# Performance work log

Measured on AMD Instinct MI355X. Metric: run time of the kernel, lower is better.

Reference implementation:

```python
import jax, jax.numpy as jnp
import numpy as np

S, B, T = 500, 128, 250          # encoder steps, batch, decoder text_len
H, K, V, VOCAB = 512, 128, 128, 1000
NEG = -1e9


def _lstm_cell(x, h, c, w_ih, w_hh, b_ih, b_hh):
    # torch.nn.LSTMCell gate order: i, f, g, o
    gates = x @ w_ih.T + b_ih + h @ w_hh.T + b_hh
    i, f, g, o = jnp.split(gates, 4, axis=-1)
    c_new = jax.nn.sigmoid(f) * c + jax.nn.sigmoid(i) * jnp.tanh(g)
    h_new = jax.nn.sigmoid(o) * jnp.tanh(c_new)
    return h_new, c_new


def setup_inputs():
    root = jax.random.key(0)
    ks = jax.random.split(root, 12)
    w = lambda k, shape, fan: (jax.random.normal(k, shape, jnp.float32) / np.sqrt(fan))
    inp = {
        'key': jax.random.normal(ks[0], (S, B, K), jnp.float32),
        'values': jax.random.normal(ks[1], (S, B, V), jnp.float32),
        'lens': jnp.maximum(jax.random.randint(ks[2], (B,), 0, S), 1),
        'text': jax.random.randint(ks[3], (T, B), 0, VOCAB),
        # embedding, padding_idx=0 -> row 0 zeroed
        'emb': w(ks[4], (VOCAB, H), H).at[0].set(0.0),
        # lstm1: input hidden_dim + value_size -> hidden H
        'w_ih1': w(ks[5], (4 * H, H + V), H + V),
        'w_hh1': w(ks[6], (4 * H, H), H),
        'b_ih1': jnp.zeros((4 * H,), jnp.float32),
        'b_hh1': jnp.zeros((4 * H,), jnp.float32),
        # lstm2: input H -> key_size K
        'w_ih2': w(ks[7], (4 * K, H), H),
        'w_hh2': w(ks[8], (4 * K, K), K),
        'b_ih2': jnp.zeros((4 * K,), jnp.float32),
        'b_hh2': jnp.zeros((4 * K,), jnp.float32),
        # character_prob: (key_size+value_size) -> vocab
        'w_out': w(ks[9], (VOCAB, K + V), K + V),
        'b_out': jnp.zeros((VOCAB,), jnp.float32),
    }
    return inp


def reference(key, values, lens, text, emb, w_ih1, w_hh1, b_ih1, b_hh1,
              w_ih2, w_hh2, b_ih2, b_hh2, w_out, b_out):
    key_t = jnp.transpose(key, (1, 0, 2))      # [B,S,K]
    val_t = jnp.transpose(values, (1, 0, 2))   # [B,S,V]
    mask = jnp.arange(S)[None, :] >= lens[:, None]  # [B,S] True = padded

    # teacher forcing ratio == 1: step 0 uses embedding(argmax(zeros)) = row 0,
    # steps i>=1 use embeddings[i]. Precompute the whole input sequence.
    embs = emb[text]  # [T,B,H]
    step0 = jnp.broadcast_to(emb[0], (1, B, H))
    char_seq = jnp.concatenate([step0, embs[1:T - 1]], axis=0)  # [T-1,B,H]

    def step(carry, char_embed):
        h1, c1, h2, c2, context = carry
        inp = jnp.concatenate([char_embed, context], axis=1)        # [B,H+V]
        h1, c1 = _lstm_cell(inp, h1, c1, w_ih1, w_hh1, b_ih1, b_hh1)
        h2, c2 = _lstm_cell(h1, h2, c2, w_ih2, w_hh2, b_ih2, b_hh2)  # query [B,K]
        energy = jnp.einsum('bsk,bk->bs', key_t, h2)
        energy = jnp.where(mask, NEG, energy)
        attn = jax.nn.softmax(energy, axis=1)
        context = jnp.einsum('bs,bsv->bv', attn, val_t)              # [B,V]
        pred = jnp.concatenate([h2, context], axis=1) @ w_out.T + b_out
        return (h1, c1, h2, c2, context), pred

    z = lambda d: jnp.zeros((B, d), jnp.float32)
    init = (z(H), z(H), z(K), z(K), z(V))
    _, preds = jax.lax.scan(step, init, char_seq)   # [T-1,B,VOCAB]
    return jnp.transpose(preds, (1, 0, 2))          # [B,T-1,VOCAB]
```

## Files before the change

kernel.cpp:

```cpp
#include <hip/hip_runtime.h>
#include <hip/hip_bf16.h>

typedef unsigned short u16;
typedef unsigned long long u64;
typedef short short8 __attribute__((ext_vector_type(8)));
typedef float f32x4 __attribute__((ext_vector_type(4)));

#define S_ 500
#define B_ 128
#define T_ 250
#define H_ 512
#define K_ 128
#define V_ 128
#define VOC 1000
#define NSTEP 249
#define NWG 160
#define NROW 128

#define VSH_BYTES   128000
#define H1ST_STRIDE 520
#define ALIAS_BYTES 33280
#define SMEM_BYTES  (VSH_BYTES + ALIAS_BYTES)

__device__ __forceinline__ float bf2f(u16 u) {
    union { unsigned int i; float f; } x; x.i = ((unsigned int)u) << 16; return x.f;
}
__device__ __forceinline__ u16 f2bf(float f) {
    union { float f; unsigned int i; } x; x.f = f;
    unsigned int r = x.i + 0x7fffu + ((x.i >> 16) & 1u);
    return (u16)(r >> 16);
}
__device__ __forceinline__ float sigm(float x) { return 1.f / (1.f + __expf(-x)); }
__device__ __forceinline__ f32x4 mfma16(short8 a, short8 b, f32x4 c) {
    return __builtin_amdgcn_mfma_f32_16x16x32_bf16(a, b, c, 0, 0, 0);
}

__device__ __forceinline__ u64 ld_state8(const u16* p) {
    return __hip_atomic_load((const u64*)p, __ATOMIC_RELAXED, __HIP_MEMORY_SCOPE_AGENT);
}
__device__ __forceinline__ short8 ld_state16(const u16* p) {
    union { u64 q[2]; short8 s; } u;
    u.q[0] = ld_state8(p); u.q[1] = ld_state8(p + 4);
    return u.s;
}
__device__ __forceinline__ unsigned ld_state4(const u16* p) {
    return __hip_atomic_load((const unsigned*)p, __ATOMIC_RELAXED, __HIP_MEMORY_SCOPE_AGENT);
}
__device__ __forceinline__ void st_state4(u16* p, unsigned v) {
    __hip_atomic_store((unsigned*)p, v, __ATOMIC_RELAXED, __HIP_MEMORY_SCOPE_AGENT);
}
__device__ __forceinline__ void st_pair(u16* p, float a, float b) {
    st_state4(p, (unsigned)f2bf(a) | ((unsigned)f2bf(b) << 16));
}

__device__ __forceinline__ void gbar(unsigned* bar, int wg) {
    __syncthreads();
    if (threadIdx.x == 0) {
        unsigned* leaf = bar + (wg & 7) * 64;
        unsigned* root = bar + 512;
        unsigned* gen  = bar + 576;
        unsigned g = __hip_atomic_load(gen, __ATOMIC_RELAXED, __HIP_MEMORY_SCOPE_AGENT);
        unsigned a = __hip_atomic_fetch_add(leaf, 1u, __ATOMIC_RELAXED, __HIP_MEMORY_SCOPE_AGENT);
        if (a == 19u) {
            __hip_atomic_store(leaf, 0u, __ATOMIC_RELAXED, __HIP_MEMORY_SCOPE_AGENT);
            unsigned r = __hip_atomic_fetch_add(root, 1u, __ATOMIC_RELAXED, __HIP_MEMORY_SCOPE_AGENT);
            if (r == 7u) {
                __hip_atomic_store(root, 0u, __ATOMIC_RELAXED, __HIP_MEMORY_SCOPE_AGENT);
                __hip_atomic_store(gen, g + 1u, __ATOMIC_RELAXED, __HIP_MEMORY_SCOPE_AGENT);
            } else {
                while (__hip_atomic_load(gen, __ATOMIC_RELAXED, __HIP_MEMORY_SCOPE_AGENT) == g)
                    __builtin_amdgcn_s_sleep(1);
            }
        } else {
            while (__hip_atomic_load(gen, __ATOMIC_RELAXED, __HIP_MEMORY_SCOPE_AGENT) == g)
                __builtin_amdgcn_s_sleep(1);
        }
    }
    __syncthreads();
}

__global__ __launch_bounds__(256) void pack_kernel(
    const float* __restrict__ w_ih1, const float* __restrict__ w_hh1,
    const float* __restrict__ b_ih1, const float* __restrict__ b_hh1,
    const float* __restrict__ w_ih2, const float* __restrict__ w_hh2,
    const float* __restrict__ b_ih2, const float* __restrict__ b_hh2,
    const float* __restrict__ w_out, const float* __restrict__ emb,
    u16* __restrict__ W1f, u16* __restrict__ W2f, u16* __restrict__ Woutf,
    float* __restrict__ bias1, float* __restrict__ bias2, u16* __restrict__ emb_bf,
    unsigned* __restrict__ bar)
{
    const int i0 = blockIdx.x * 256 + threadIdx.x;
    const int stride = gridDim.x * 256;
    for (int i = i0; i < 1024; i += stride)
        __hip_atomic_store(bar + i, 0u, __ATOMIC_RELAXED, __HIP_MEMORY_SCOPE_AGENT);
    for (int i = i0; i < 1152 * 2048; i += stride) {
        int k = i >> 11, n = i & 2047;
        float v = (k < 640) ? w_ih1[n * 640 + k] : w_hh1[n * 512 + (k - 640)];
        W1f[((size_t)(k >> 3) * 2048 + n) * 8 + (k & 7)] = f2bf(v);
    }
    for (int i = i0; i < 640 * 512; i += stride) {
        int k = i >> 9, n = i & 511;
        float v = (k < 512) ? w_ih2[n * 512 + k] : w_hh2[n * 128 + (k - 512)];
        W2f[((size_t)(k >> 3) * 512 + n) * 8 + (k & 7)] = f2bf(v);
    }
    for (int i = i0; i < 256 * 1024; i += stride) {
        int k = i >> 10, n = i & 1023;
        float v = (n < VOC) ? w_out[n * 256 + k] : 0.f;
        Woutf[((size_t)(k >> 3) * 1024 + n) * 8 + (k & 7)] = f2bf(v);
    }
    for (int i = i0; i < 2048; i += stride) bias1[i] = b_ih1[i] + b_hh1[i];
    for (int i = i0; i < 512; i += stride) bias2[i] = b_ih2[i] + b_hh2[i];
    for (int i = i0; i < VOC * H_; i += stride) emb_bf[i] = f2bf(emb[i]);
}

__global__ __launch_bounds__(256) void conv_kv_kernel(
    const float* __restrict__ key, const float* __restrict__ values,
    u16* __restrict__ key_bf, u16* __restrict__ val_bf)
{
    const int i0 = blockIdx.x * 256 + threadIdx.x;
    const int stride = gridDim.x * 256;
    for (int i = i0; i < S_ * B_ * K_; i += stride) {
        int s = i >> 14;
        int r = i & 16383;
        int b = r >> 7, k = r & 127;
        size_t d = ((size_t)b * S_ + s) * K_ + k;
        key_bf[d] = f2bf(key[i]);
        val_bf[d] = f2bf(values[i]);
    }
}

__global__ __launch_bounds__(256, 1) void decoder_kernel(
    const u16* __restrict__ emb_bf, const int* __restrict__ text,
    const u16* __restrict__ W1f, const float* __restrict__ bias1,
    const u16* __restrict__ W2f, const float* __restrict__ bias2,
    const u16* __restrict__ key_bf, const u16* __restrict__ val_bf,
    const int* __restrict__ lens,
    u16* __restrict__ CT, u16* __restrict__ H1, u16* __restrict__ H2,
    u16* __restrict__ Hc, unsigned* __restrict__ bar)
{
    extern __shared__ char smem[];
    u16*   vshare = (u16*)smem;
    char*  alias  = smem + VSH_BYTES;
    u16*   h1st   = (u16*)alias;
    float* Gb     = (float*)alias;
    float* ebuf   = (float*)alias;
    float* cbuf   = (float*)(alias + 2048);
    float* h2s    = (float*)(alias + 4096);
    float* redm   = (float*)(alias + 4608);

    const int wg = blockIdx.x;
    const int tid = threadIdx.x;
    const int lane = tid & 63, wv = tid >> 6;
    const int lrow = lane & 15, lk = lane >> 4;
    const bool isrow = wg < NROW;

    const int mh1 = wg >> 5, hg1 = wg & 31;
    const int n1 = wv * 512 + hg1 * 16 + lrow;
    const int l2 = wg - NROW;
    const int q2 = l2 >> 3, hg2 = l2 & 7;
    const int n2 = wv * 128 + hg2 * 16 + lrow;
    const int b  = wg;
    const int mylen = isrow ? lens[b] : 0;

    float c1r[2] = {0.f, 0.f};
    float c2r[2] = {0.f, 0.f};
    f32x4 acc1[2] = {{0,0,0,0},{0,0,0,0}};
    f32x4 acc2[2] = {{0,0,0,0},{0,0,0,0}};

    {
        int i0 = wg * 256 + tid, stride = NWG * 256;
        for (int i = i0; i < B_ * V_ / 2; i += stride) st_state4(CT + 2 * i, 0u);
        for (int i = i0; i < B_ * H_ / 2; i += stride) st_state4(H1 + 2 * i, 0u);
        for (int i = i0; i < B_ * K_;     i += stride) st_state4(H2 + 2 * i, 0u);
        if (isrow) {
            const u16* vp = val_bf + (size_t)b * S_ * V_;
            for (int i = tid; i < (S_ * V_) / 8; i += 256)
                *reinterpret_cast<short8*>(vshare + i * 8) =
                    *reinterpret_cast<const short8*>(vp + (size_t)i * 8);
        }
    }
    gbar(bar, wg);

    for (int t = 0; t < NSTEP; ++t) {
        const int nxt = (t & 1) ^ 1;
        u16* H2n = H2 + (size_t)nxt * B_ * K_;

        if (isrow) {
            int grow[2];
#pragma unroll
            for (int rt = 0; rt < 2; ++rt) grow[rt] = mh1 * 32 + rt * 16 + lrow;
#pragma unroll
            for (int kc = 16; kc < 20; ++kc) {
                int k = kc * 32 + lk * 8;
                short8 bw = *reinterpret_cast<const short8*>(W1f + ((size_t)(k >> 3) * 2048 + n1) * 8);
#pragma unroll
                for (int rt = 0; rt < 2; ++rt) {
                    short8 a = ld_state16(CT + grow[rt] * V_ + (k - 512));
                    acc1[rt] = mfma16(a, bw, acc1[rt]);
                }
            }
            float bv = bias1[n1];
#pragma unroll
            for (int rt = 0; rt < 2; ++rt)
#pragma unroll
                for (int j = 0; j < 4; ++j)
                    Gb[(rt * 16 + lk * 4 + j) * 65 + wv * 16 + lrow] = acc1[rt][j] + bv;
            __syncthreads();
            {
                int rb = tid >> 3, j0 = (tid & 7) * 2;
                int bb = mh1 * 32 + rb;
                float gi0 = Gb[rb * 65 + j0],      gf0 = Gb[rb * 65 + 16 + j0];
                float gg0 = Gb[rb * 65 + 32 + j0], go0 = Gb[rb * 65 + 48 + j0];
                float gi1 = Gb[rb * 65 + j0 + 1],      gf1 = Gb[rb * 65 + 16 + j0 + 1];
                float gg1 = Gb[rb * 65 + 32 + j0 + 1], go1 = Gb[rb * 65 + 48 + j0 + 1];
                float cn0 = sigm(gf0) * c1r[0] + sigm(gi0) * tanhf(gg0);
                float cn1 = sigm(gf1) * c1r[1] + sigm(gi1) * tanhf(gg1);
                c1r[0] = cn0; c1r[1] = cn1;
                st_pair(H1 + bb * H_ + hg1 * 16 + j0,
                        sigm(go0) * tanhf(cn0), sigm(go1) * tanhf(cn1));
            }
        }
        gbar(bar, wg);

        if (isrow) {
            {
                const u16* src = H1 + (size_t)(mh1 * 32) * H_;
#pragma unroll
                for (int it = 0; it < 8; ++it) {
                    int c = it * 256 + tid;
                    int row = c >> 6, col = (c & 63) * 8;
                    u64 lo = ld_state8(src + (size_t)row * H_ + col);
                    u64 hi = ld_state8(src + (size_t)row * H_ + col + 4);
                    u64* dst = (u64*)(h1st + row * H1ST_STRIDE + col);
                    dst[0] = lo; dst[1] = hi;
                }
            }
            const u16* aemb[2];
#pragma unroll
            for (int rt = 0; rt < 2; ++rt) {
                int grow = mh1 * 32 + rt * 16 + lrow;
                int tok = text[(t + 1) * B_ + grow];
                aemb[rt] = emb_bf + (size_t)tok * H_;
            }
            __syncthreads();
            acc1[0] = (f32x4){0,0,0,0}; acc1[1] = (f32x4){0,0,0,0};
#pragma unroll 4
            for (int kc = 0; kc < 16; ++kc) {
                int k = kc * 32 + lk * 8;
                short8 bw = *reinterpret_cast<const short8*>(W1f + ((size_t)(k >> 3) * 2048 + n1) * 8);
#pragma unroll
                for (int rt = 0; rt < 2; ++rt) {
                    short8 a = *reinterpret_cast<const short8*>(aemb[rt] + k);
                    acc1[rt] = mfma16(a, bw, acc1[rt]);
                }
            }
#pragma unroll 4
            for (int kc = 20; kc < 36; ++kc) {
                int k = kc * 32 + lk * 8;
                short8 bw = *reinterpret_cast<const short8*>(W1f + ((size_t)(k >> 3) * 2048 + n1) * 8);
#pragma unroll
                for (int rt = 0; rt < 2; ++rt) {
                    short8 a = *reinterpret_cast<const short8*>(
                        h1st + (rt * 16 + lrow) * H1ST_STRIDE + (kc - 20) * 32 + lk * 8);
                    acc1[rt] = mfma16(a, bw, acc1[rt]);
                }
            }
        } else {
            {
                const u16* src = H1 + (size_t)(q2 * 32) * H_;
#pragma unroll
                for (int it = 0; it < 8; ++it) {
                    int c = it * 256 + tid;
                    int row = c >> 6, col = (c & 63) * 8;
                    u64 lo = ld_state8(src + (size_t)row * H_ + col);
                    u64 hi = ld_state8(src + (size_t)row * H_ + col + 4);
                    u64* dst = (u64*)(h1st + row * H1ST_STRIDE + col);
                    dst[0] = lo; dst[1] = hi;
                }
            }
            __syncthreads();
#pragma unroll 4
            for (int kc = 0; kc < 16; ++kc) {
                int k = kc * 32 + lk * 8;
                short8 bw = *reinterpret_cast<const short8*>(W2f + ((size_t)(k >> 3) * 512 + n2) * 8);
#pragma unroll
                for (int rt = 0; rt < 2; ++rt) {
                    short8 a = *reinterpret_cast<const short8*>(
                        h1st + (rt * 16 + lrow) * H1ST_STRIDE + kc * 32 + lk * 8);
                    acc2[rt] = mfma16(a, bw, acc2[rt]);
                }
            }
            float bv = bias2[n2];
            __syncthreads();
#pragma unroll
            for (int rt = 0; rt < 2; ++rt)
#pragma unroll
                for (int j = 0; j < 4; ++j)
                    Gb[(rt * 16 + lk * 4 + j) * 65 + wv * 16 + lrow] = acc2[rt][j] + bv;
            __syncthreads();
            {
                int rb = tid >> 3, j0 = (tid & 7) * 2;
                int bb = q2 * 32 + rb;
                float gi0 = Gb[rb * 65 + j0],      gf0 = Gb[rb * 65 + 16 + j0];
                float gg0 = Gb[rb * 65 + 32 + j0], go0 = Gb[rb * 65 + 48 + j0];
                float gi1 = Gb[rb * 65 + j0 + 1],      gf1 = Gb[rb * 65 + 16 + j0 + 1];
                float gg1 = Gb[rb * 65 + 32 + j0 + 1], go1 = Gb[rb * 65 + 48 + j0 + 1];
                float cn0 = sigm(gf0) * c2r[0] + sigm(gi0) * tanhf(gg0);
                float cn1 = sigm(gf1) * c2r[1] + sigm(gi1) * tanhf(gg1);
                c2r[0] = cn0; c2r[1] = cn1;
                st_pair(H2n + bb * K_ + hg2 * 16 + j0,
                        sigm(go0) * tanhf(cn0), sigm(go1) * tanhf(cn1));
            }
        }
        gbar(bar, wg);

        if (isrow) {
            u16* Hc_t = Hc + (size_t)t * B_ * 256;
            if (tid < 64) {
                unsigned v = ld_state4(H2n + b * K_ + 2 * tid);
                h2s[2 * tid]     = bf2f((u16)(v & 0xffffu));
                h2s[2 * tid + 1] = bf2f((u16)(v >> 16));
                *reinterpret_cast<unsigned*>(Hc_t + b * 256 + 2 * tid) = v;
            }
            __syncthreads();

            for (int s = tid; s < 512; s += 256) {
                float e = -1e9f;
                if (s < S_) {
                    const u16* kp = key_bf + ((size_t)b * S_ + s) * K_;
                    float a = 0.f;
#pragma unroll
                    for (int kk = 0; kk < K_; kk += 8) {
                        short8 kv = *reinterpret_cast<const short8*>(kp + kk);
#pragma unroll
                        for (int j = 0; j < 8; ++j)
                            a += bf2f((u16)kv[j]) * h2s[kk + j];
                    }
                    e = (s < mylen) ? a : -1e9f;
                }
                ebuf[s] = e;
            }
            __syncthreads();

            float m = fmaxf(ebuf[tid], ebuf[tid + 256]);
#pragma unroll
            for (int off = 32; off > 0; off >>= 1) m = fmaxf(m, __shfl_down(m, off));
            if (lane == 0) redm[wv] = m;
            __syncthreads();
            const float maxv = fmaxf(fmaxf(redm[0], redm[1]), fmaxf(redm[2], redm[3]));

            float psum = 0.f;
            for (int s = tid; s < 512; s += 256) {
                float pv = __expf(ebuf[s] - maxv);
                ebuf[s] = pv;
                psum += pv;
            }
#pragma unroll
            for (int off = 32; off > 0; off >>= 1) psum += __shfl_down(psum, off);
            if (lane == 0) redm[4 + wv] = psum;
            __syncthreads();
            const float rinv = 1.f / (redm[4] + redm[5] + redm[6] + redm[7]);

            const int s0 = wv * 125;
            float p0 = 0.f, p1 = 0.f;
            for (int s = s0; s < s0 + 125; ++s) {
                float w = ebuf[s];
                unsigned pk = *reinterpret_cast<const unsigned*>(vshare + s * V_ + lane * 2);
                p0 += w * bf2f((u16)(pk & 0xffffu));
                p1 += w * bf2f((u16)(pk >> 16));
            }
            cbuf[wv * V_ + lane * 2]     = p0;
            cbuf[wv * V_ + lane * 2 + 1] = p1;
            __syncthreads();

            if (tid < 64) {
                int v0 = 2 * tid, v1 = 2 * tid + 1;
                float ctx0 = (cbuf[v0] + cbuf[V_ + v0] + cbuf[2 * V_ + v0] + cbuf[3 * V_ + v0]) * rinv;
                float ctx1 = (cbuf[v1] + cbuf[V_ + v1] + cbuf[2 * V_ + v1] + cbuf[3 * V_ + v1]) * rinv;
                st_pair(CT + b * V_ + v0, ctx0, ctx1);
                *reinterpret_cast<unsigned*>(Hc_t + b * 256 + K_ + v0) =
                    (unsigned)f2bf(ctx0) | ((unsigned)f2bf(ctx1) << 16);
            }
        } else {
            acc2[0] = (f32x4){0,0,0,0}; acc2[1] = (f32x4){0,0,0,0};
#pragma unroll
            for (int kc = 16; kc < 20; ++kc) {
                int k = kc * 32 + lk * 8;
                short8 bw = *reinterpret_cast<const short8*>(W2f + ((size_t)(k >> 3) * 512 + n2) * 8);
#pragma unroll
                for (int rt = 0; rt < 2; ++rt) {
                    short8 a = ld_state16(H2n + (q2 * 32 + rt * 16 + lrow) * K_ + (k - 512));
                    acc2[rt] = mfma16(a, bw, acc2[rt]);
                }
            }
        }
        gbar(bar, wg);
    }
}

__global__ __launch_bounds__(256) void k4_kernel(
    const u16* __restrict__ Hc, const u16* __restrict__ Woutf,
    const float* __restrict__ b_out, float* __restrict__ out)
{
    const int bx = blockIdx.x;
    const int mt = bx >> 4, nt = bx & 15;
    const int tid = threadIdx.x;
    const int lane = tid & 63, g = tid >> 6;
    const int lrow = lane & 15, lk = lane >> 4;
    const int n = nt * 64 + g * 16 + lrow;
    const float bias = (n < VOC) ? b_out[n] : 0.f;

    f32x4 acc[8];
#pragma unroll
    for (int rt = 0; rt < 8; ++rt) acc[rt] = (f32x4){bias, bias, bias, bias};

#pragma unroll
    for (int kc = 0; kc < 8; ++kc) {
        int k = kc * 32 + lk * 8;
        short8 bw = *reinterpret_cast<const short8*>(Woutf + ((size_t)(k >> 3) * 1024 + n) * 8);
#pragma unroll
        for (int rt = 0; rt < 8; ++rt) {
            int R = mt * 128 + rt * 16 + lrow;
            short8 a = *reinterpret_cast<const short8*>(Hc + (size_t)R * 256 + k);
            acc[rt] = mfma16(a, bw, acc[rt]);
        }
    }
    if (n < VOC) {
#pragma unroll
        for (int rt = 0; rt < 8; ++rt)
#pragma unroll
            for (int j = 0; j < 4; ++j) {
                int R = mt * 128 + rt * 16 + lk * 4 + j;
                int tt = R >> 7, bb = R & 127;
                out[((size_t)bb * NSTEP + tt) * VOC + n] = acc[rt][j];
            }
    }
}

extern "C" void kernel_launch(void* const* d_in, const int* in_sizes, int n_in,
                              void* d_out, int out_size, void* d_ws, size_t ws_size,
                              hipStream_t stream)
{
    const float* key    = (const float*)d_in[0];
    const float* values = (const float*)d_in[1];
    const int*   lens   = (const int*)d_in[2];
    const int*   text   = (const int*)d_in[3];
    const float* emb    = (const float*)d_in[4];
    const float* w_ih1  = (const float*)d_in[5];
    const float* w_hh1  = (const float*)d_in[6];
    const float* b_ih1  = (const float*)d_in[7];
    const float* b_hh1  = (const float*)d_in[8];
    const float* w_ih2  = (const float*)d_in[9];
    const float* w_hh2  = (const float*)d_in[10];
    const float* b_ih2  = (const float*)d_in[11];
    const float* b_hh2  = (const float*)d_in[12];
    const float* w_out  = (const float*)d_in[13];
    const float* b_out  = (const float*)d_in[14];

    char* p = (char*)d_ws;
    auto alloc = [&](size_t bytes) -> char* {
        char* r = p;
        p += (bytes + 255) & ~(size_t)255;
        return r;
    };
    u16*      key_bf = (u16*)     alloc((size_t)B_ * S_ * K_ * 2);
    u16*      val_bf = (u16*)     alloc((size_t)B_ * S_ * V_ * 2);
    u16*      emb_bf = (u16*)     alloc((size_t)VOC * H_ * 2);
    u16*      W1f    = (u16*)     alloc((size_t)1152 * 2048 * 2);
    u16*      W2f    = (u16*)     alloc((size_t)640 * 512 * 2);
    u16*      Woutf  = (u16*)     alloc((size_t)256 * 1024 * 2);
    float*    bias1  = (float*)   alloc(2048 * 4);
    float*    bias2  = (float*)   alloc(512 * 4);
    u16*      CT     = (u16*)     alloc((size_t)B_ * V_ * 2);
    u16*      H1     = (u16*)     alloc((size_t)B_ * H_ * 2);
    u16*      H2     = (u16*)     alloc((size_t)2 * B_ * K_ * 2);
    u16*      Hc     = (u16*)     alloc((size_t)NSTEP * B_ * 256 * 2);
    unsigned* bar    = (unsigned*)alloc(4096);
    (void)ws_size; (void)in_sizes; (void)n_in; (void)out_size;

    hipFuncSetAttribute((const void*)decoder_kernel,
                        hipFuncAttributeMaxDynamicSharedMemorySize, SMEM_BYTES);

    pack_kernel<<<512, 256, 0, stream>>>(w_ih1, w_hh1, b_ih1, b_hh1,
                                         w_ih2, w_hh2, b_ih2, b_hh2,
                                         w_out, emb, W1f, W2f, Woutf, bias1, bias2, emb_bf,
                                         bar);
    conv_kv_kernel<<<4096, 256, 0, stream>>>(key, values, key_bf, val_bf);

    decoder_kernel<<<NWG, 256, SMEM_BYTES, stream>>>(emb_bf, text, W1f, bias1, W2f, bias2,
                                                     key_bf, val_bf, lens, CT, H1, H2, Hc, bar);

    k4_kernel<<<NSTEP * 16, 256, 0, stream>>>(Hc, Woutf, b_out, (float*)d_out);
}
```

Before: 6.308 ms.

## Fold LSTM2 into per-batch row workgroups to remove a grid barrier per step

Drops the 32 dedicated LSTM2 workgroups. Each of the 128 batch-row workgroups now computes its own row's second LSTM cell with scalar FMA dot products over a regate-packed W2 layout, keeping h2 in shared memory. This removes one grid-wide barrier per decoder step and the global H2 round trip. The embedding part of the LSTM1 GEMM is also moved ahead of the barrier to overlap with the wait. In exchange, each workgroup streams the full W2 matrix every step with non-MFMA math, which adds per-step latency on the critical path.

```diff
diff --git a/kernel.cpp b/kernel.cpp
--- a/kernel.cpp
+++ b/kernel.cpp
@@ -14,13 +14,14 @@
 #define V_ 128
 #define VOC 1000
 #define NSTEP 249
-#define NWG 160
-#define NROW 128
-
-#define VSH_BYTES   128000
-#define H1ST_STRIDE 520
-#define ALIAS_BYTES 33280
-#define SMEM_BYTES  (VSH_BYTES + ALIAS_BYTES)
+#define NWG 128
+
+#define H1ST_STRIDE 516
+#define OFF_H1ST   128000
+#define OFF_EBUF   (OFF_H1ST + 33024)
+#define OFF_H2S    (OFF_EBUF + 2048)
+#define OFF_REDM   (OFF_H2S + 512)
+#define SMEM_BYTES (OFF_REDM + 64)
 
 __device__ __forceinline__ float bf2f(u16 u) {
     union { unsigned int i; float f; } x; x.i = ((unsigned int)u) << 16; return x.f;
@@ -42,9 +43,6 @@
     union { u64 q[2]; short8 s; } u;
     u.q[0] = ld_state8(p); u.q[1] = ld_state8(p + 4);
     return u.s;
-}
-__device__ __forceinline__ unsigned ld_state4(const u16* p) {
-    return __hip_atomic_load((const unsigned*)p, __ATOMIC_RELAXED, __HIP_MEMORY_SCOPE_AGENT);
 }
 __device__ __forceinline__ void st_state4(u16* p, unsigned v) {
     __hip_atomic_store((unsigned*)p, v, __ATOMIC_RELAXED, __HIP_MEMORY_SCOPE_AGENT);
@@ -61,7 +59,7 @@
         unsigned* gen  = bar + 576;
         unsigned g = __hip_atomic_load(gen, __ATOMIC_RELAXED, __HIP_MEMORY_SCOPE_AGENT);
         unsigned a = __hip_atomic_fetch_add(leaf, 1u, __ATOMIC_RELAXED, __HIP_MEMORY_SCOPE_AGENT);
-        if (a == 19u) {
+        if (a == 15u) {
             __hip_atomic_store(leaf, 0u, __ATOMIC_RELAXED, __HIP_MEMORY_SCOPE_AGENT);
             unsigned r = __hip_atomic_fetch_add(root, 1u, __ATOMIC_RELAXED, __HIP_MEMORY_SCOPE_AGENT);
             if (r == 7u) {
@@ -85,8 +83,8 @@
     const float* __restrict__ w_ih2, const float* __restrict__ w_hh2,
     const float* __restrict__ b_ih2, const float* __restrict__ b_hh2,
     const float* __restrict__ w_out, const float* __restrict__ emb,
-    u16* __restrict__ W1f, u16* __restrict__ W2f, u16* __restrict__ Woutf,
-    float* __restrict__ bias1, float* __restrict__ bias2, u16* __restrict__ emb_bf,
+    u16* __restrict__ W1f, u16* __restrict__ W2gp, u16* __restrict__ Woutf,
+    float* __restrict__ bias1, float* __restrict__ bias2p, u16* __restrict__ emb_bf,
     unsigned* __restrict__ bar)
 {
     const int i0 = blockIdx.x * 256 + threadIdx.x;
@@ -101,7 +99,14 @@
     for (int i = i0; i < 640 * 512; i += stride) {
         int k = i >> 9, n = i & 511;
         float v = (k < 512) ? w_ih2[n * 512 + k] : w_hh2[n * 128 + (k - 512)];
-        W2f[((size_t)(k >> 3) * 512 + n) * 8 + (k & 7)] = f2bf(v);
+        int d = n & 127, g = n >> 7;
+        int t = (g >> 1) * 128 + d, slot = g & 1;
+        W2gp[((size_t)k * 256 + t) * 2 + slot] = f2bf(v);
+    }
+    for (int i = i0; i < 512; i += stride) {
+        int d = i & 127, g = i >> 7;
+        int t = (g >> 1) * 128 + d, slot = g & 1;
+        bias2p[t * 2 + slot] = b_ih2[i] + b_hh2[i];
     }
     for (int i = i0; i < 256 * 1024; i += stride) {
         int k = i >> 10, n = i & 1023;
@@ -109,7 +114,6 @@
         Woutf[((size_t)(k >> 3) * 1024 + n) * 8 + (k & 7)] = f2bf(v);
     }
     for (int i = i0; i < 2048; i += stride) bias1[i] = b_ih1[i] + b_hh1[i];
-    for (int i = i0; i < 512; i += stride) bias2[i] = b_ih2[i] + b_hh2[i];
     for (int i = i0; i < VOC * H_; i += stride) emb_bf[i] = f2bf(emb[i]);
 }
 
@@ -132,60 +136,50 @@
 __global__ __launch_bounds__(256, 1) void decoder_kernel(
     const u16* __restrict__ emb_bf, const int* __restrict__ text,
     const u16* __restrict__ W1f, const float* __restrict__ bias1,
-    const u16* __restrict__ W2f, const float* __restrict__ bias2,
+    const u16* __restrict__ W2gp, const float* __restrict__ bias2p,
     const u16* __restrict__ key_bf, const u16* __restrict__ val_bf,
     const int* __restrict__ lens,
-    u16* __restrict__ CT, u16* __restrict__ H1, u16* __restrict__ H2,
+    u16* __restrict__ CT, u16* __restrict__ H1,
     u16* __restrict__ Hc, unsigned* __restrict__ bar)
 {
     extern __shared__ char smem[];
     u16*   vshare = (u16*)smem;
-    char*  alias  = smem + VSH_BYTES;
-    u16*   h1st   = (u16*)alias;
-    float* Gb     = (float*)alias;
-    float* ebuf   = (float*)alias;
-    float* cbuf   = (float*)(alias + 2048);
-    float* h2s    = (float*)(alias + 4096);
-    float* redm   = (float*)(alias + 4608);
+    u16*   h1st   = (u16*)(smem + OFF_H1ST);
+    float* Gb     = (float*)(smem + OFF_H1ST);
+    float* ebuf   = (float*)(smem + OFF_EBUF);
+    float* h2s    = (float*)(smem + OFF_H2S);
+    float* redm   = (float*)(smem + OFF_REDM);
 
     const int wg = blockIdx.x;
     const int tid = threadIdx.x;
     const int lane = tid & 63, wv = tid >> 6;
     const int lrow = lane & 15, lk = lane >> 4;
-    const bool isrow = wg < NROW;
 
     const int mh1 = wg >> 5, hg1 = wg & 31;
     const int n1 = wv * 512 + hg1 * 16 + lrow;
-    const int l2 = wg - NROW;
-    const int q2 = l2 >> 3, hg2 = l2 & 7;
-    const int n2 = wv * 128 + hg2 * 16 + lrow;
     const int b  = wg;
-    const int mylen = isrow ? lens[b] : 0;
+    const int mylen = lens[b];
+    const int gd  = tid & 127;
+    const int pgo = tid >> 7;
 
     float c1r[2] = {0.f, 0.f};
-    float c2r[2] = {0.f, 0.f};
+    float c2r = 0.f;
     f32x4 acc1[2] = {{0,0,0,0},{0,0,0,0}};
-    f32x4 acc2[2] = {{0,0,0,0},{0,0,0,0}};
 
     {
         int i0 = wg * 256 + tid, stride = NWG * 256;
         for (int i = i0; i < B_ * V_ / 2; i += stride) st_state4(CT + 2 * i, 0u);
         for (int i = i0; i < B_ * H_ / 2; i += stride) st_state4(H1 + 2 * i, 0u);
-        for (int i = i0; i < B_ * K_;     i += stride) st_state4(H2 + 2 * i, 0u);
-        if (isrow) {
-            const u16* vp = val_bf + (size_t)b * S_ * V_;
-            for (int i = tid; i < (S_ * V_) / 8; i += 256)
-                *reinterpret_cast<short8*>(vshare + i * 8) =
-                    *reinterpret_cast<const short8*>(vp + (size_t)i * 8);
-        }
+        if (tid < 128) h2s[tid] = 0.f;
+        const u16* vp = val_bf + (size_t)b * S_ * V_;
+        for (int i = tid; i < (S_ * V_) / 8; i += 256)
+            *reinterpret_cast<short8*>(vshare + i * 8) =
+                *reinterpret_cast<const short8*>(vp + (size_t)i * 8);
     }
     gbar(bar, wg);
 
     for (int t = 0; t < NSTEP; ++t) {
-        const int nxt = (t & 1) ^ 1;
-        u16* H2n = H2 + (size_t)nxt * B_ * K_;
-
-        if (isrow) {
+        {
             int grow[2];
 #pragma unroll
             for (int rt = 0; rt < 2; ++rt) grow[rt] = mh1 * 32 + rt * 16 + lrow;
@@ -219,10 +213,27 @@
                 st_pair(H1 + bb * H_ + hg1 * 16 + j0,
                         sigm(go0) * tanhf(cn0), sigm(go1) * tanhf(cn1));
             }
+            acc1[0] = (f32x4){0,0,0,0}; acc1[1] = (f32x4){0,0,0,0};
+            const u16* aemb[2];
+#pragma unroll
+            for (int rt = 0; rt < 2; ++rt) {
+                int tok = text[(t + 1) * B_ + grow[rt]];
+                aemb[rt] = emb_bf + (size_t)tok * H_;
+            }
+#pragma unroll 4
+            for (int kc = 0; kc < 16; ++kc) {
+                int k = kc * 32 + lk * 8;
+                short8 bw = *reinterpret_cast<const short8*>(W1f + ((size_t)(k >> 3) * 2048 + n1) * 8);
+#pragma unroll
+                for (int rt = 0; rt < 2; ++rt) {
+                    short8 a = *reinterpret_cast<const short8*>(aemb[rt] + k);
+                    acc1[rt] = mfma16(a, bw, acc1[rt]);
+                }
+            }
         }
         gbar(bar, wg);
 
-        if (isrow) {
+        {
             {
                 const u16* src = H1 + (size_t)(mh1 * 32) * H_;
 #pragma unroll
@@ -235,92 +246,41 @@
                     dst[0] = lo; dst[1] = hi;
                 }
             }
-            const u16* aemb[2];
-#pragma unroll
-            for (int rt = 0; rt < 2; ++rt) {
-                int grow = mh1 * 32 + rt * 16 + lrow;
-                int tok = text[(t + 1) * B_ + grow];
-                aemb[rt] = emb_bf + (size_t)tok * H_;
-            }
-            __syncthreads();
-            acc1[0] = (f32x4){0,0,0,0}; acc1[1] = (f32x4){0,0,0,0};
-#pragma unroll 4
-            for (int kc = 0; kc < 16; ++kc) {
-                int k = kc * 32 + lk * 8;
-                short8 bw = *reinterpret_cast<const short8*>(W1f + ((size_t)(k >> 3) * 2048 + n1) * 8);
-#pragma unroll
-                for (int rt = 0; rt < 2; ++rt) {
-                    short8 a = *reinterpret_cast<const short8*>(aemb[rt] + k);
-                    acc1[rt] = mfma16(a, bw, acc1[rt]);
-                }
-            }
-#pragma unroll 4
-            for (int kc = 20; kc < 36; ++kc) {
-                int k = kc * 32 + lk * 8;
-                short8 bw = *reinterpret_cast<const short8*>(W1f + ((size_t)(k >> 3) * 2048 + n1) * 8);
-#pragma unroll
-                for (int rt = 0; rt < 2; ++rt) {
-                    short8 a = *reinterpret_cast<const short8*>(
-                        h1st + (rt * 16 + lrow) * H1ST_STRIDE + (kc - 20) * 32 + lk * 8);
-                    acc1[rt] = mfma16(a, bw, acc1[rt]);
-                }
-            }
-        } else {
+            __syncthreads();
+
+            float accA = bias2p[tid * 2], accB = bias2p[tid * 2 + 1];
             {
-                const u16* src = H1 + (size_t)(q2 * 32) * H_;
-#pragma unroll
-                for (int it = 0; it < 8; ++it) {
-                    int c = it * 256 + tid;
-                    int row = c >> 6, col = (c & 63) * 8;
-                    u64 lo = ld_state8(src + (size_t)row * H_ + col);
-                    u64 hi = ld_state8(src + (size_t)row * H_ + col + 4);
-                    u64* dst = (u64*)(h1st + row * H1ST_STRIDE + col);
-                    dst[0] = lo; dst[1] = hi;
-                }
-            }
-            __syncthreads();
-#pragma unroll 4
-            for (int kc = 0; kc < 16; ++kc) {
-                int k = kc * 32 + lk * 8;
-                short8 bw = *reinterpret_cast<const short8*>(W2f + ((size_t)(k >> 3) * 512 + n2) * 8);
-#pragma unroll
-                for (int rt = 0; rt < 2; ++rt) {
-                    short8 a = *reinterpret_cast<const short8*>(
-                        h1st + (rt * 16 + lrow) * H1ST_STRIDE + kc * 32 + lk * 8);
-                    acc2[rt] = mfma16(a, bw, acc2[rt]);
-                }
-            }
-            float bv = bias2[n2];
-            __syncthreads();
-#pragma unroll
-            for (int rt = 0; rt < 2; ++rt)
-#pragma unroll
-                for (int j = 0; j < 4; ++j)
-                    Gb[(rt * 16 + lk * 4 + j) * 65 + wv * 16 + lrow] = acc2[rt][j] + bv;
-            __syncthreads();
-            {
-                int rb = tid >> 3, j0 = (tid & 7) * 2;
-                int bb = q2 * 32 + rb;
-                float gi0 = Gb[rb * 65 + j0],      gf0 = Gb[rb * 65 + 16 + j0];
-                float gg0 = Gb[rb * 65 + 32 + j0], go0 = Gb[rb * 65 + 48 + j0];
-                float gi1 = Gb[rb * 65 + j0 + 1],      gf1 = Gb[rb * 65 + 16 + j0 + 1];
-                float gg1 = Gb[rb * 65 + 32 + j0 + 1], go1 = Gb[rb * 65 + 48 + j0 + 1];
-                float cn0 = sigm(gf0) * c2r[0] + sigm(gi0) * tanhf(gg0);
-                float cn1 = sigm(gf1) * c2r[1] + sigm(gi1) * tanhf(gg1);
-                c2r[0] = cn0; c2r[1] = cn1;
-                st_pair(H2n + bb * K_ + hg2 * 16 + j0,
-                        sigm(go0) * tanhf(cn0), sigm(go1) * tanhf(cn1));
-            }
-        }
-        gbar(bar, wg);
-
-        if (isrow) {
+                const u16* h1row = h1st + (b & 31) * H1ST_STRIDE;
+#pragma unroll 8
+                for (int k = 0; k < 512; k += 2) {
+                    unsigned hv = *reinterpret_cast<const unsigned*>(h1row + k);
+                    float a0 = bf2f((u16)(hv & 0xffffu));
+                    float a1 = bf2f((u16)(hv >> 16));
+                    unsigned w0 = *reinterpret_cast<const unsigned*>(W2gp + ((size_t)k * 256 + tid) * 2);
+                    unsigned w1 = *reinterpret_cast<const unsigned*>(W2gp + ((size_t)(k + 1) * 256 + tid) * 2);
+                    accA += a0 * bf2f((u16)(w0 & 0xffffu));
+                    accB += a0 * bf2f((u16)(w0 >> 16));
+                    accA += a1 * bf2f((u16)(w1 & 0xffffu));
+                    accB += a1 * bf2f((u16)(w1 >> 16));
+                }
+#pragma unroll 8
+                for (int k = 512; k < 640; ++k) {
+                    float a = h2s[k - 512];
+                    unsigned w = *reinterpret_cast<const unsigned*>(W2gp + ((size_t)k * 256 + tid) * 2);
+                    accA += a * bf2f((u16)(w & 0xffffu));
+                    accB += a * bf2f((u16)(w >> 16));
+                }
+            }
             u16* Hc_t = Hc + (size_t)t * B_ * 256;
-            if (tid < 64) {
-                unsigned v = ld_state4(H2n + b * K_ + 2 * tid);
-                h2s[2 * tid]     = bf2f((u16)(v & 0xffffu));
-                h2s[2 * tid + 1] = bf2f((u16)(v >> 16));
-                *reinterpret_cast<unsigned*>(Hc_t + b * 256 + 2 * tid) = v;
+            if (pgo) { ebuf[gd] = accA; ebuf[128 + gd] = accB; }
+            __syncthreads();
+            if (!pgo) {
+                float gg = ebuf[gd], go = ebuf[128 + gd];
+                float cn = sigm(accB) * c2r + sigm(accA) * tanhf(gg);
+                c2r = cn;
+                float hn = sigm(go) * tanhf(cn);
+                h2s[gd] = hn;
+                Hc_t[b * 256 + gd] = f2bf(hn);
             }
             __syncthreads();
 
@@ -369,6 +329,8 @@
                 p0 += w * bf2f((u16)(pk & 0xffffu));
                 p1 += w * bf2f((u16)(pk >> 16));
             }
+            __syncthreads();
+            float* cbuf = ebuf;
             cbuf[wv * V_ + lane * 2]     = p0;
             cbuf[wv * V_ + lane * 2 + 1] = p1;
             __syncthreads();
@@ -381,16 +343,16 @@
                 *reinterpret_cast<unsigned*>(Hc_t + b * 256 + K_ + v0) =
                     (unsigned)f2bf(ctx0) | ((unsigned)f2bf(ctx1) << 16);
             }
-        } else {
-            acc2[0] = (f32x4){0,0,0,0}; acc2[1] = (f32x4){0,0,0,0};
-#pragma unroll
-            for (int kc = 16; kc < 20; ++kc) {
+
+#pragma unroll 4
+            for (int kc = 20; kc < 36; ++kc) {
                 int k = kc * 32 + lk * 8;
-                short8 bw = *reinterpret_cast<const short8*>(W2f + ((size_t)(k >> 3) * 512 + n2) * 8);
+                short8 bw = *reinterpret_cast<const short8*>(W1f + ((size_t)(k >> 3) * 2048 + n1) * 8);
 #pragma unroll
                 for (int rt = 0; rt < 2; ++rt) {
-                    short8 a = ld_state16(H2n + (q2 * 32 + rt * 16 + lrow) * K_ + (k - 512));
-                    acc2[rt] = mfma16(a, bw, acc2[rt]);
+                    short8 a = *reinterpret_cast<const short8*>(
+                        h1st + (rt * 16 + lrow) * H1ST_STRIDE + (kc - 20) * 32 + lk * 8);
+                    acc1[rt] = mfma16(a, bw, acc1[rt]);
                 }
             }
         }
@@ -467,13 +429,12 @@
     u16*      val_bf = (u16*)     alloc((size_t)B_ * S_ * V_ * 2);
     u16*      emb_bf = (u16*)     alloc((size_t)VOC * H_ * 2);
     u16*      W1f    = (u16*)     alloc((size_t)1152 * 2048 * 2);
-    u16*      W2f    = (u16*)     alloc((size_t)640 * 512 * 2);
+    u16*      W2gp   = (u16*)     alloc((size_t)640 * 512 * 2);
     u16*      Woutf  = (u16*)     alloc((size_t)256 * 1024 * 2);
     float*    bias1  = (float*)   alloc(2048 * 4);
-    float*    bias2  = (float*)   alloc(512 * 4);
+    float*    bias2p = (float*)   alloc(512 * 4);
     u16*      CT     = (u16*)     alloc((size_t)B_ * V_ * 2);
     u16*      H1     = (u16*)     alloc((size_t)B_ * H_ * 2);
-    u16*      H2     = (u16*)     alloc((size_t)2 * B_ * K_ * 2);
     u16*      Hc     = (u16*)     alloc((size_t)NSTEP * B_ * 256 * 2);
     unsigned* bar    = (unsigned*)alloc(4096);
     (void)ws_size; (void)in_sizes; (void)n_in; (void)out_size;
@@ -483,12 +444,12 @@
 
     pack_kernel<<<512, 256, 0, stream>>>(w_ih1, w_hh1, b_ih1, b_hh1,
                                          w_ih2, w_hh2, b_ih2, b_hh2,
-                                         w_out, emb, W1f, W2f, Woutf, bias1, bias2, emb_bf,
+                                         w_out, emb, W1f, W2gp, Woutf, bias1, bias2p, emb_bf,
                                          bar);
     conv_kv_kernel<<<4096, 256, 0, stream>>>(key, values, key_bf, val_bf);
 
-    decoder_kernel<<<NWG, 256, SMEM_BYTES, stream>>>(emb_bf, text, W1f, bias1, W2f, bias2,
-                                                     key_bf, val_bf, lens, CT, H1, H2, Hc, bar);
+    decoder_kernel<<<NWG, 256, SMEM_BYTES, stream>>>(emb_bf, text, W1f, bias1, W2gp, bias2p,
+                                                     key_bf, val_bf, lens, CT, H1, Hc, bar);
 
     k4_kernel<<<NSTEP * 16, 256, 0, stream>>>(Hc, Woutf, b_out, (float*)d_out);
 }
```

Result: slower. 17.47 ms (+176.9%).

## Replace tree grid barrier with per-workgroup flag barrier and fast tanh

Applied to the files above, without the earlier changes.

Swaps the two-level atomic counter grid barrier for a flag array: each workgroup stores a monotonically increasing tag to its own slot, and 160 threads in each workgroup poll all slots in parallel until every one has reached the tag. This removes the serialized atomic fetch-adds, the leaf and root resets and the sleep-based polling on the critical path of the roughly thousand barriers per launch. In exchange every barrier now issues many more polling loads. Separately, tanhf is replaced with an exp-based formula that is cheaper but slightly less accurate.

```diff
diff --git a/kernel.cpp b/kernel.cpp
--- a/kernel.cpp
+++ b/kernel.cpp
@@ -31,6 +31,7 @@
     return (u16)(r >> 16);
 }
 __device__ __forceinline__ float sigm(float x) { return 1.f / (1.f + __expf(-x)); }
+__device__ __forceinline__ float tanh_f(float x) { return 2.f / (1.f + __expf(-2.f * x)) - 1.f; }
 __device__ __forceinline__ f32x4 mfma16(short8 a, short8 b, f32x4 c) {
     return __builtin_amdgcn_mfma_f32_16x16x32_bf16(a, b, c, 0, 0, 0);
 }
@@ -53,28 +54,13 @@
     st_state4(p, (unsigned)f2bf(a) | ((unsigned)f2bf(b) << 16));
 }
 
-__device__ __forceinline__ void gbar(unsigned* bar, int wg) {
+__device__ __forceinline__ void gbar(unsigned* flags, int wg, unsigned tag) {
     __syncthreads();
-    if (threadIdx.x == 0) {
-        unsigned* leaf = bar + (wg & 7) * 64;
-        unsigned* root = bar + 512;
-        unsigned* gen  = bar + 576;
-        unsigned g = __hip_atomic_load(gen, __ATOMIC_RELAXED, __HIP_MEMORY_SCOPE_AGENT);
-        unsigned a = __hip_atomic_fetch_add(leaf, 1u, __ATOMIC_RELAXED, __HIP_MEMORY_SCOPE_AGENT);
-        if (a == 19u) {
-            __hip_atomic_store(leaf, 0u, __ATOMIC_RELAXED, __HIP_MEMORY_SCOPE_AGENT);
-            unsigned r = __hip_atomic_fetch_add(root, 1u, __ATOMIC_RELAXED, __HIP_MEMORY_SCOPE_AGENT);
-            if (r == 7u) {
-                __hip_atomic_store(root, 0u, __ATOMIC_RELAXED, __HIP_MEMORY_SCOPE_AGENT);
-                __hip_atomic_store(gen, g + 1u, __ATOMIC_RELAXED, __HIP_MEMORY_SCOPE_AGENT);
-            } else {
-                while (__hip_atomic_load(gen, __ATOMIC_RELAXED, __HIP_MEMORY_SCOPE_AGENT) == g)
-                    __builtin_amdgcn_s_sleep(1);
-            }
-        } else {
-            while (__hip_atomic_load(gen, __ATOMIC_RELAXED, __HIP_MEMORY_SCOPE_AGENT) == g)
-                __builtin_amdgcn_s_sleep(1);
-        }
+    if (threadIdx.x == 0)
+        __hip_atomic_store(flags + wg, tag, __ATOMIC_RELAXED, __HIP_MEMORY_SCOPE_AGENT);
+    if (threadIdx.x < NWG) {
+        while (__hip_atomic_load(flags + threadIdx.x, __ATOMIC_RELAXED,
+                                 __HIP_MEMORY_SCOPE_AGENT) < tag) {}
     }
     __syncthreads();
 }
@@ -166,6 +152,7 @@
     float c2r[2] = {0.f, 0.f};
     f32x4 acc1[2] = {{0,0,0,0},{0,0,0,0}};
     f32x4 acc2[2] = {{0,0,0,0},{0,0,0,0}};
+    unsigned tag = 1;
 
     {
         int i0 = wg * 256 + tid, stride = NWG * 256;
@@ -179,7 +166,7 @@
                     *reinterpret_cast<const short8*>(vp + (size_t)i * 8);
         }
     }
-    gbar(bar, wg);
+    gbar(bar, wg, tag++);
 
     for (int t = 0; t < NSTEP; ++t) {
         const int nxt = (t & 1) ^ 1;
@@ -213,14 +200,14 @@
                 float gg0 = Gb[rb * 65 + 32 + j0], go0 = Gb[rb * 65 + 48 + j0];
                 float gi1 = Gb[rb * 65 + j0 + 1],      gf1 = Gb[rb * 65 + 16 + j0 + 1];
                 float gg1 = Gb[rb * 65 + 32 + j0 + 1], go1 = Gb[rb * 65 + 48 + j0 + 1];
-                float cn0 = sigm(gf0) * c1r[0] + sigm(gi0) * tanhf(gg0);
-                float cn1 = sigm(gf1) * c1r[1] + sigm(gi1) * tanhf(gg1);
+                float cn0 = sigm(gf0) * c1r[0] + sigm(gi0) * tanh_f(gg0);
+                float cn1 = sigm(gf1) * c1r[1] + sigm(gi1) * tanh_f(gg1);
                 c1r[0] = cn0; c1r[1] = cn1;
                 st_pair(H1 + bb * H_ + hg1 * 16 + j0,
-                        sigm(go0) * tanhf(cn0), sigm(go1) * tanhf(cn1));
+                        sigm(go0) * tanh_f(cn0), sigm(go1) * tanh_f(cn1));
             }
         }
-        gbar(bar, wg);
+        gbar(bar, wg, tag++);
 
         if (isrow) {
             {
@@ -305,14 +292,14 @@
                 float gg0 = Gb[rb * 65 + 32 + j0], go0 = Gb[rb * 65 + 48 + j0];
                 float gi1 = Gb[rb * 65 + j0 + 1],      gf1 = Gb[rb * 65 + 16 + j0 + 1];
                 float gg1 = Gb[rb * 65 + 32 + j0 + 1], go1 = Gb[rb * 65 + 48 + j0 + 1];
-                float cn0 = sigm(gf0) * c2r[0] + sigm(gi0) * tanhf(gg0);
-                float cn1 = sigm(gf1) * c2r[1] + sigm(gi1) * tanhf(gg1);
+                float cn0 = sigm(gf0) * c2r[0] + sigm(gi0) * tanh_f(gg0);
+                float cn1 = sigm(gf1) * c2r[1] + sigm(gi1) * tanh_f(gg1);
                 c2r[0] = cn0; c2r[1] = cn1;
                 st_pair(H2n + bb * K_ + hg2 * 16 + j0,
-                        sigm(go0) * tanhf(cn0), sigm(go1) * tanhf(cn1));
+                        sigm(go0) * tanh_f(cn0), sigm(go1) * tanh_f(cn1));
             }
         }
-        gbar(bar, wg);
+        gbar(bar, wg, tag++);
 
         if (isrow) {
             u16* Hc_t = Hc + (size_t)t * B_ * 256;
@@ -394,7 +381,7 @@
                 }
             }
         }
-        gbar(bar, wg);
+        gbar(bar, wg, tag++);
     }
 }
 
```

Result: slower. 7.661 ms (+21.4%).
